# Kernel tuning notes

Hardware: AMD Instinct MI355X
Metric: run time of the kernel (lower is better)

Reference implementation:

```python
import jax, jax.numpy as jnp
import numpy as np

N, E, G = 50000, 800000, 64
L, C, IN, H, OUT = 3, 4, 64, 64, 64
BN_EPS = 1e-5


def setup_inputs() -> dict:
    key = jax.random.key(0)
    ks = jax.random.split(key, 12)
    x = jax.random.normal(ks[0], (N, IN), dtype=jnp.float32)
    cluster_labels = jax.random.randint(ks[1], (N,), 0, C, dtype=jnp.int32)
    edge_index = jax.random.randint(ks[2], (2, E), 0, N, dtype=jnp.int64)
    batch = jnp.sort(jax.random.randint(ks[3], (N,), 0, G, dtype=jnp.int64))
    s1 = 1.0 / np.sqrt(H)
    # per (layer, cluster) GIN MLP params: Lin(H,H) -> BN -> ReLU -> Lin(H,H)
    W1 = jax.random.normal(ks[4], (L, C, H, H), dtype=jnp.float32) * s1
    b1 = jnp.zeros((L, C, H), dtype=jnp.float32)
    g1 = jnp.ones((L, C, H), dtype=jnp.float32)
    be1 = jnp.zeros((L, C, H), dtype=jnp.float32)
    W2 = jax.random.normal(ks[5], (L, C, H, H), dtype=jnp.float32) * s1
    b2 = jnp.zeros((L, C, H), dtype=jnp.float32)
    # pool MLP: Lin(H*L, H) -> BN -> ReLU -> Lin(H, OUT)
    Wp1 = jax.random.normal(ks[6], (H * L, H), dtype=jnp.float32) / np.sqrt(H * L)
    bp1 = jnp.zeros((H,), dtype=jnp.float32)
    gp = jnp.ones((H,), dtype=jnp.float32)
    bep = jnp.zeros((H,), dtype=jnp.float32)
    Wp2 = jax.random.normal(ks[7], (H, OUT), dtype=jnp.float32) * s1
    bp2 = jnp.zeros((OUT,), dtype=jnp.float32)
    return {"x": x, "cluster_labels": cluster_labels, "edge_index": edge_index,
            "batch": batch, "W1": W1, "b1": b1, "g1": g1, "be1": be1,
            "W2": W2, "b2": b2, "Wp1": Wp1, "bp1": bp1, "gp": gp,
            "bep": bep, "Wp2": Wp2, "bp2": bp2}


def _masked_bn(h, mf, gamma, beta):
    # BatchNorm computed only over rows where mask is set (those are the rows fed to nn)
    cnt = jnp.maximum(mf.sum(), 1.0)
    mean = (mf[:, None] * h).sum(0) / cnt
    var = (mf[:, None] * (h - mean) ** 2).sum(0) / cnt
    return (h - mean) * jax.lax.rsqrt(var + BN_EPS) * gamma + beta


def _bn(h, gamma, beta):
    mean = h.mean(0)
    var = ((h - mean) ** 2).mean(0)
    return (h - mean) * jax.lax.rsqrt(var + BN_EPS) * gamma + beta


def reference(x, cluster_labels, edge_index, batch, W1, b1, g1, be1, W2, b2,
              Wp1, bp1, gp, bep, Wp2, bp2):
    src, dst = edge_index[0], edge_index[1]
    pooled = []
    for t in range(L):
        for c in range(C):
            mask = cluster_labels == c
            mf = mask.astype(x.dtype)
            # GIN aggregation: out[i] = sum_{j -> i} x[j]
            agg = jax.ops.segment_sum(x[src], dst, num_segments=N)
            h = agg + x  # (1 + eps) * x residual with eps = 0
            h = h @ W1[t, c] + b1[t, c]
            h = jax.nn.relu(_masked_bn(h, mf, g1[t, c], be1[t, c]))
            h = h @ W2[t, c] + b2[t, c]
            x = jnp.where(mask[:, None], h, x)
        pooled.append(jax.ops.segment_sum(x, batch, num_segments=G))
    z = jnp.concatenate(pooled, axis=1)  # [G, H*L]
    z = z @ Wp1 + bp1
    z = jax.nn.relu(_bn(z, gp, bep))
    return z @ Wp2 + bp2
```

## Files before the change

### kernel.cpp

```cpp
#include <hip/hip_runtime.h>
#include <hip/hip_bf16.h>

#define NN 50000
#define EE 800000
#define GG 64
#define LL 3
#define CC 4
#define HH 64
#define BN_EPS 1e-5f
#define NSHADOW 4
#define SBLK 196
#define GIN_BLOCKS 2048
#define MM_BLOCKS 256
#define ECHUNKS 3125
#define NODE_RANGE 6250


typedef __attribute__((ext_vector_type(8))) short bf16x8;
typedef __attribute__((ext_vector_type(4))) float f32x4;

__device__ __forceinline__ float bf2f(short s) {
    return __int_as_float(((int)(unsigned short)s) << 16);
}
__device__ __forceinline__ short f2bf(float v) {
    __hip_bfloat16 hb = __float2bfloat16(v);
    return *(short*)&hb;
}


__global__ void k_deghist(const int* __restrict__ dst, int* __restrict__ deg,
                          const int* __restrict__ labels, int* __restrict__ blockcnt,
                          const float* __restrict__ x_in, __hip_bfloat16* __restrict__ xw,
                          const float* __restrict__ W1, const float* __restrict__ W2,
                          short* __restrict__ wf) {
    __shared__ int cnt[CC];
    int tid = threadIdx.x;
    for (int i = blockIdx.x * 256 + tid; i < NN * 64; i += gridDim.x * 256)
        xw[i] = __float2bfloat16(x_in[i]);
    int o = blockIdx.x * 256 + tid;
    if (o < 24 * 4096) {
        int m = o >> 12;
        int r = o & 4095;
        int colt = r >> 10;
        int fragk = (r >> 9) & 1;
        int lane = (r >> 3) & 63;
        int j = r & 7;
        int k = fragk * 32 + ((lane >> 4) << 3) + j;
        int n = colt * 16 + (lane & 15);
        const float* src = (m < 12) ? (W1 + (size_t)m * 4096) : (W2 + (size_t)(m - 12) * 4096);
        wf[o] = f2bf(src[k * 64 + n]);
    }
    bool hist = (blockIdx.x < SBLK);
    if (hist && tid < CC) cnt[tid] = 0;
    __syncthreads();
    int gid = blockIdx.x * 256 + tid;
    if (gid < EE) atomicAdd(&deg[dst[gid]], 1);
    if (hist && gid < NN) atomicAdd(&cnt[labels[gid]], 1);
    __syncthreads();
    if (hist && tid < CC) blockcnt[tid * SBLK + blockIdx.x] = cnt[tid];
}

__global__ __launch_bounds__(256) void k_scancombo(
    const int* __restrict__ deg, int* __restrict__ rowptr, int* __restrict__ dpart,
    const int* __restrict__ blockcnt, int* __restrict__ coffs, int* __restrict__ ccount) {
    __shared__ int smem[CC * 256];
    int tid = threadIdx.x;
    if (blockIdx.x < SBLK) {
        int i = blockIdx.x * 256 + tid;
        int v = (i < NN) ? deg[i] : 0;
        smem[tid] = v;
        __syncthreads();
        for (int off = 1; off < 256; off <<= 1) {
            int u = (tid >= off) ? smem[tid - off] : 0;
            __syncthreads();
            smem[tid] += u;
            __syncthreads();
        }
        if (i < NN) rowptr[i] = smem[tid] - v;
        if (tid == 255) dpart[blockIdx.x] = smem[255];
    } else {
        int own[CC];
        for (int c = 0; c < CC; c++) {
            own[c] = (tid < SBLK) ? blockcnt[c * SBLK + tid] : 0;
            smem[c * 256 + tid] = own[c];
        }
        __syncthreads();
        for (int off = 1; off < 256; off <<= 1) {
            int v[CC];
            for (int c = 0; c < CC; c++) v[c] = (tid >= off) ? smem[c * 256 + tid - off] : 0;
            __syncthreads();
            for (int c = 0; c < CC; c++) smem[c * 256 + tid] += v[c];
            __syncthreads();
        }
        if (tid < SBLK)
            for (int c = 0; c < CC; c++) coffs[c * SBLK + tid] = smem[c * 256 + tid] - own[c];
        if (tid == 0)
            for (int c = 0; c < CC; c++) ccount[c] = smem[c * 256 + 255];
    }
}

__global__ __launch_bounds__(256) void k_dscan2(int* __restrict__ dpart,
                                                int* __restrict__ dbase,
                                                int* __restrict__ rowptr) {
    __shared__ int s[256];
    int tid = threadIdx.x;
    int v = (tid < SBLK) ? dpart[tid] : 0;
    s[tid] = v;
    __syncthreads();
    for (int off = 1; off < 256; off <<= 1) {
        int u = (tid >= off) ? s[tid - off] : 0;
        __syncthreads();
        s[tid] += u;
        __syncthreads();
    }
    if (tid < SBLK) dbase[tid] = s[tid] - v;
    if (tid == 0) rowptr[NN] = EE;
}

__global__ __launch_bounds__(256) void k_cfill_dscan3(
    int* __restrict__ rowptr, const int* __restrict__ dbase, int* __restrict__ cursor,
    const int* __restrict__ labels, const int* __restrict__ coffs, int* __restrict__ clist) {
    __shared__ int pos[CC];
    int tid = threadIdx.x;
    if (tid < CC) pos[tid] = coffs[tid * SBLK + blockIdx.x];
    __syncthreads();
    int i = blockIdx.x * 256 + tid;
    if (i < NN) {
        int r = rowptr[i] + dbase[blockIdx.x];
        rowptr[i] = r;
        cursor[i] = r;
        int c = labels[i];
        int p = atomicAdd(&pos[c], 1);
        clist[c * NN + p] = i;
    }
}

__global__ void k_fill(const int* __restrict__ src, const int* __restrict__ dst,
                       int* __restrict__ cursor, int* __restrict__ adj) {
    int range = blockIdx.x / ECHUNKS;
    int e = (blockIdx.x - range * ECHUNKS) * 256 + threadIdx.x;
    if (e < EE) {
        int d = dst[e];
        int lo = range * NODE_RANGE;
        if (d >= lo && d < lo + NODE_RANGE) {
            int pos = atomicAdd(&cursor[d], 1);
            adj[pos] = src[e] << 7;
        }
    }
}

__global__ __launch_bounds__(256) void k_gather(
    const __hip_bfloat16* __restrict__ xw, const int* __restrict__ adj,
    const int* __restrict__ rowptr, const int* __restrict__ clist_c,
    const int* __restrict__ ccount_c, __hip_bfloat16* __restrict__ aggbuf,
    const int* __restrict__ batch, float* __restrict__ z, int tpool) {
    int cnt = *ccount_c;
    int lane = threadIdx.x & 63;
    int wave = threadIdx.x >> 6;
    int wid = blockIdx.x * 4 + wave;
    int nwaves = gridDim.x * 4;
    int grp = lane >> 4;
    int l16 = lane & 15;
    const char* xwb = (const char*)xw;
    int idx = wid;
    int node_next = (idx < cnt) ? clist_c[idx] : 0;
    for (; idx < cnt; idx += nwaves) {
        int node = node_next;
        int nidx = idx + nwaves;
        if (nidx < cnt) node_next = clist_c[nidx];
        int rb = rowptr[node], re = rowptr[node + 1];
        float ax[8], ay[8], az[8], aw[8];
        #pragma unroll
        for (int u = 0; u < 8; u++) { ax[u] = 0.f; ay[u] = 0.f; az[u] = 0.f; aw[u] = 0.f; }
        if (grp == 0) {
            uint2 v = *(const uint2*)(xwb + ((size_t)node << 7) + l16 * 8);
            ax[0] += __int_as_float((int)(v.x << 16));
            ay[0] += __int_as_float((int)(v.x & 0xffff0000u));
            az[0] += __int_as_float((int)(v.y << 16));
            aw[0] += __int_as_float((int)(v.y & 0xffff0000u));
        }
        int base = rb, rem = re - rb;
        while (rem > 0) {
            int take = min(rem, 64);
            int nb = adj[base + min(lane, take - 1)];
            int j = 0;
            for (; j + 32 <= take; j += 32) {
                #pragma unroll
                for (int u = 0; u < 8; u++) {
                    int o = __shfl(nb, j + u * 4 + grp);
                    uint2 v = *(const uint2*)(xwb + o + l16 * 8);
                    ax[u] += __int_as_float((int)(v.x << 16));
                    ay[u] += __int_as_float((int)(v.x & 0xffff0000u));
                    az[u] += __int_as_float((int)(v.y << 16));
                    aw[u] += __int_as_float((int)(v.y & 0xffff0000u));
                }
            }
            for (; j + 16 <= take; j += 16) {
                #pragma unroll
                for (int u = 0; u < 4; u++) {
                    int o = __shfl(nb, j + u * 4 + grp);
                    uint2 v = *(const uint2*)(xwb + o + l16 * 8);
                    ax[u] += __int_as_float((int)(v.x << 16));
                    ay[u] += __int_as_float((int)(v.x & 0xffff0000u));
                    az[u] += __int_as_float((int)(v.y << 16));
                    aw[u] += __int_as_float((int)(v.y & 0xffff0000u));
                }
            }
            for (; j < take; j += 4) {
                int e = j + grp;
                int o = __shfl(nb, min(e, take - 1));
                if (e < take) {
                    uint2 v = *(const uint2*)(xwb + o + l16 * 8);
                    ax[0] += __int_as_float((int)(v.x << 16));
                    ay[0] += __int_as_float((int)(v.x & 0xffff0000u));
                    az[0] += __int_as_float((int)(v.y << 16));
                    aw[0] += __int_as_float((int)(v.y & 0xffff0000u));
                }
            }
            base += take; rem -= take;
        }
        float X = ((ax[0] + ax[1]) + (ax[2] + ax[3])) + ((ax[4] + ax[5]) + (ax[6] + ax[7]));
        float Y = ((ay[0] + ay[1]) + (ay[2] + ay[3])) + ((ay[4] + ay[5]) + (ay[6] + ay[7]));
        float Z = ((az[0] + az[1]) + (az[2] + az[3])) + ((az[4] + az[5]) + (az[6] + az[7]));
        float W = ((aw[0] + aw[1]) + (aw[2] + aw[3])) + ((aw[4] + aw[5]) + (aw[6] + aw[7]));
        X += __shfl_xor(X, 16); X += __shfl_xor(X, 32);
        Y += __shfl_xor(Y, 16); Y += __shfl_xor(Y, 32);
        Z += __shfl_xor(Z, 16); Z += __shfl_xor(Z, 32);
        W += __shfl_xor(W, 16); W += __shfl_xor(W, 32);
        if (grp == 0) {
            ushort4 st;
            st.x = (unsigned short)f2bf(X);
            st.y = (unsigned short)f2bf(Y);
            st.z = (unsigned short)f2bf(Z);
            st.w = (unsigned short)f2bf(W);
            *(ushort4*)((char*)aggbuf + ((size_t)idx << 7) + l16 * 8) = st;
        }
    }
    if (tpool >= 0) {
        int lo = wid * 64;
        if (lo < NN) {
            int hi = min(lo + 64, NN);
            float acc = 0.f;
            int curg = batch[lo];
            for (int n = lo; n < hi; n++) {
                int g = batch[n];
                if (g != curg) {
                    atomicAdd(&z[curg * (HH * LL) + tpool * HH + lane], acc);
                    acc = 0.f;
                    curg = g;
                }
                acc += __bfloat162float(xw[(size_t)n * 64 + lane]);
            }
            atomicAdd(&z[curg * (HH * LL) + tpool * HH + lane], acc);
        }
    }
}

__global__ __launch_bounds__(256) void k_lin1(
    const __hip_bfloat16* __restrict__ aggbuf, const int* __restrict__ ccount_c,
    const short* __restrict__ wf1, const float* __restrict__ b1c,
    __hip_bfloat16* __restrict__ h1buf, float* __restrict__ bnacc) {
    int cnt = *ccount_c;
    int tiles = (cnt + 15) >> 4;
    int lane = threadIdx.x & 63;
    int wave = threadIdx.x >> 6;
    int wid = blockIdx.x * 4 + wave;
    int nwaves = gridDim.x * 4;
    int quad = lane >> 4;
    int l15 = lane & 15;

    bf16x8 wb[8];
    #pragma unroll
    for (int f = 0; f < 8; f++)
        wb[f] = *(const bf16x8*)(wf1 + f * 512 + lane * 8);
    float bcol[4];
    #pragma unroll
    for (int colt = 0; colt < 4; colt++) bcol[colt] = b1c[colt * 16 + l15];

    float sS[4] = {0.f, 0.f, 0.f, 0.f};
    float sQ[4] = {0.f, 0.f, 0.f, 0.f};

    for (int tile = wid; tile < tiles; tile += nwaves) {
        int tb = tile << 4;
        int row = tb + l15;
        const __hip_bfloat16* ar = aggbuf + (size_t)row * 64 + quad * 8;
        bf16x8 a0 = *(const bf16x8*)ar;
        bf16x8 a1 = *(const bf16x8*)(ar + 32);
        #pragma unroll
        for (int colt = 0; colt < 4; colt++) {
            f32x4 acc = {0.f, 0.f, 0.f, 0.f};
            acc = __builtin_amdgcn_mfma_f32_16x16x32_bf16(a0, wb[colt * 2 + 0], acc, 0, 0, 0);
            acc = __builtin_amdgcn_mfma_f32_16x16x32_bf16(a1, wb[colt * 2 + 1], acc, 0, 0, 0);
            #pragma unroll
            for (int r = 0; r < 4; r++) {
                int nrow = tb + quad * 4 + r;
                if (nrow < cnt) {
                    float s = acc[r] + bcol[colt];
                    __hip_bfloat16 hb = __float2bfloat16(s);
                    h1buf[(size_t)nrow * 64 + colt * 16 + l15] = hb;
                    float st = __bfloat162float(hb);
                    sS[colt] += st;
                    sQ[colt] += st * st;
                }
            }
        }
    }
    #pragma unroll
    for (int colt = 0; colt < 4; colt++) {
        sS[colt] += __shfl_xor(sS[colt], 16); sS[colt] += __shfl_xor(sS[colt], 32);
        sQ[colt] += __shfl_xor(sQ[colt], 16); sQ[colt] += __shfl_xor(sQ[colt], 32);
    }
    if (quad == 0) {
        int slot = (blockIdx.x & (NSHADOW - 1)) * 128;
        #pragma unroll
        for (int colt = 0; colt < 4; colt++) {
            atomicAdd(&bnacc[slot + colt * 16 + l15], sS[colt]);
            atomicAdd(&bnacc[slot + 64 + colt * 16 + l15], sQ[colt]);
        }
    }
}

__global__ __launch_bounds__(256) void k_cmfma(
    __hip_bfloat16* __restrict__ xw, const int* __restrict__ clist_c,
    const int* __restrict__ ccount_c, const float* __restrict__ g1c,
    const float* __restrict__ be1c, const short* __restrict__ wf2,
    const float* __restrict__ b2c, const __hip_bfloat16* __restrict__ h1buf,
    const float* __restrict__ bnacc) {
    __shared__ float lds_scale[64];
    __shared__ float lds_shift[64];
    int cnt = *ccount_c;
    int tiles = (cnt + 15) >> 4;
    int lane = threadIdx.x & 63;
    int wave = threadIdx.x >> 6;
    int wid = blockIdx.x * 4 + wave;
    int nwaves = gridDim.x * 4;
    int quad = lane >> 4;
    int l15 = lane & 15;

    if (threadIdx.x < 64) {
        float s = 0.f, q = 0.f;
        #pragma unroll
        for (int sh = 0; sh < NSHADOW; sh++) {
            s += bnacc[sh * 128 + threadIdx.x];
            q += bnacc[sh * 128 + 64 + threadIdx.x];
        }
        float fc = fmaxf((float)cnt, 1.f);
        float mean = s / fc;
        float var = q / fc - mean * mean;
        float sc = g1c[threadIdx.x] * rsqrtf(var + BN_EPS);
        lds_scale[threadIdx.x] = sc;
        lds_shift[threadIdx.x] = be1c[threadIdx.x] - mean * sc;
    }
    __syncthreads();

    bf16x8 wb[8];
    #pragma unroll
    for (int f = 0; f < 8; f++)
        wb[f] = *(const bf16x8*)(wf2 + f * 512 + lane * 8);
    float bcol[4];
    #pragma unroll
    for (int colt = 0; colt < 4; colt++) bcol[colt] = b2c[colt * 16 + l15];
    float scl0[8], sft0[8], scl1[8], sft1[8];
    #pragma unroll
    for (int j = 0; j < 8; j++) {
        int ch = quad * 8 + j;
        scl0[j] = lds_scale[ch];      sft0[j] = lds_shift[ch];
        scl1[j] = lds_scale[ch + 32]; sft1[j] = lds_shift[ch + 32];
    }

    for (int tile = wid; tile < tiles; tile += nwaves) {
        int tb = tile << 4;
        int row = tb + l15;
        const __hip_bfloat16* hr = h1buf + (size_t)row * 64 + quad * 8;
        bf16x8 h0 = *(const bf16x8*)hr;
        bf16x8 h1f = *(const bf16x8*)(hr + 32);
        bf16x8 a0, a1;
        #pragma unroll
        for (int j = 0; j < 8; j++) {
            a0[j] = f2bf(fmaxf(bf2f(h0[j]) * scl0[j] + sft0[j], 0.f));
            a1[j] = f2bf(fmaxf(bf2f(h1f[j]) * scl1[j] + sft1[j], 0.f));
        }
        #pragma unroll
        for (int colt = 0; colt < 4; colt++) {
            f32x4 acc = {0.f, 0.f, 0.f, 0.f};
            acc = __builtin_amdgcn_mfma_f32_16x16x32_bf16(a0, wb[colt * 2 + 0], acc, 0, 0, 0);
            acc = __builtin_amdgcn_mfma_f32_16x16x32_bf16(a1, wb[colt * 2 + 1], acc, 0, 0, 0);
            #pragma unroll
            for (int r = 0; r < 4; r++) {
                int nrow = tb + quad * 4 + r;
                if (nrow < cnt) {
                    int node = clist_c[nrow];
                    xw[(size_t)node * 64 + colt * 16 + l15] =
                        __float2bfloat16(acc[r] + bcol[colt]);
                }
            }
        }
    }
}

__global__ void k_pool(const __hip_bfloat16* __restrict__ xw, const int* __restrict__ batch,
                       float* __restrict__ z, int t) {
    const int CHUNK = 64;
    int lane = threadIdx.x & 63;
    int wg = (blockIdx.x * blockDim.x + threadIdx.x) >> 6;
    int lo = wg * CHUNK;
    if (lo >= NN) return;
    int hi = min(lo + CHUNK, NN);
    float acc = 0.f;
    int curg = batch[lo];
    for (int n = lo; n < hi; n++) {
        int g = batch[n];
        if (g != curg) {
            atomicAdd(&z[curg * (HH * LL) + t * HH + lane], acc);
            acc = 0.f;
            curg = g;
        }
        acc += __bfloat162float(xw[(size_t)n * 64 + lane]);
    }
    atomicAdd(&z[curg * (HH * LL) + t * HH + lane], acc);
}

__global__ __launch_bounds__(256) void k_final1(
    const float* __restrict__ z, const float* __restrict__ Wp1,
    const float* __restrict__ bp1, float* __restrict__ hbuf) {
    __shared__ float red[256];
    int g = blockIdx.x;
    int k = threadIdx.x & 63;
    int part = threadIdx.x >> 6;
    float s = 0.f;
    #pragma unroll 8
    for (int j = part * 48; j < (part + 1) * 48; j++)
        s += z[g * (HH * LL) + j] * Wp1[j * 64 + k];
    red[threadIdx.x] = s;
    __syncthreads();
    if (part == 0)
        hbuf[g * 64 + k] = red[k] + red[64 + k] + red[128 + k] + red[192 + k] + bp1[k];
}

__global__ __launch_bounds__(256) void k_final2(
    const float* __restrict__ hbuf, const float* __restrict__ gp,
    const float* __restrict__ bep, const float* __restrict__ Wp2,
    const float* __restrict__ bp2, float* __restrict__ out) {
    __shared__ float lds[64 * 64];
    __shared__ float sscale[64];
    __shared__ float sshift[64];
    int tid = threadIdx.x;
    for (int i = tid; i < 64 * 64; i += 256) lds[i] = hbuf[i];
    __syncthreads();
    if (tid < 64) {
        float s = 0.f, q = 0.f;
        for (int g = 0; g < 64; g++) { float v = lds[g * 64 + tid]; s += v; q += v * v; }
        float mean = s / 64.f;
        float var = q / 64.f - mean * mean;
        float sc = gp[tid] * rsqrtf(var + BN_EPS);
        sscale[tid] = sc;
        sshift[tid] = bep[tid] - mean * sc;
    }
    __syncthreads();
    for (int i = tid; i < 64 * 64; i += 256) {
        int k = i & 63;
        lds[i] = fmaxf(lds[i] * sscale[k] + sshift[k], 0.f);
    }
    __syncthreads();
    for (int i = tid; i < 64 * 64; i += 256) {
        int g = i >> 6, o = i & 63;
        float s = bp2[o];
        #pragma unroll 8
        for (int k = 0; k < 64; k++) s += lds[g * 64 + k] * Wp2[k * 64 + o];
        out[g * 64 + o] = s;
    }
}

extern "C" void kernel_launch(void* const* d_in, const int* in_sizes, int n_in,
                              void* d_out, int out_size, void* d_ws, size_t ws_size,
                              hipStream_t stream) {
    const float* x_in = (const float*)d_in[0];
    const int* labels = (const int*)d_in[1];
    const int* esrc = (const int*)d_in[2];
    const int* edst = esrc + EE;
    const int* batch = (const int*)d_in[3];
    const float* W1 = (const float*)d_in[4];
    const float* b1 = (const float*)d_in[5];
    const float* g1 = (const float*)d_in[6];
    const float* be1 = (const float*)d_in[7];
    const float* W2 = (const float*)d_in[8];
    const float* b2 = (const float*)d_in[9];
    const float* Wp1 = (const float*)d_in[10];
    const float* bp1 = (const float*)d_in[11];
    const float* gp = (const float*)d_in[12];
    const float* bep = (const float*)d_in[13];
    const float* Wp2 = (const float*)d_in[14];
    const float* bp2 = (const float*)d_in[15];
    float* out = (float*)d_out;

    char* p = (char*)d_ws;
    auto carve = [&](size_t bytes) -> void* {
        void* r = (void*)p;
        p += (bytes + 255) & ~(size_t)255;
        return r;
    };
    float* bnacc = (float*)carve((size_t)LL * CC * NSHADOW * 128 * 4);
    float* z     = (float*)carve((size_t)GG * HH * LL * 4);
    int*   deg   = (int*)carve((size_t)NN * 4);
    size_t zero_bytes = (size_t)(p - (char*)d_ws);
    int*   ccount  = (int*)carve(CC * 4);
    int*   blockcnt= (int*)carve((size_t)CC * SBLK * 4);
    int*   coffs   = (int*)carve((size_t)CC * SBLK * 4);
    int*   dpart   = (int*)carve((size_t)SBLK * 4);
    int*   dbase   = (int*)carve((size_t)SBLK * 4);
    __hip_bfloat16* xw     = (__hip_bfloat16*)carve((size_t)NN * 64 * 2);
    __hip_bfloat16* aggbuf = (__hip_bfloat16*)carve((size_t)NN * 64 * 2);
    __hip_bfloat16* h1buf  = (__hip_bfloat16*)carve((size_t)NN * 64 * 2);
    short* wf      = (short*)carve((size_t)24 * 4096 * 2);
    float* hbuf    = (float*)carve((size_t)GG * 64 * 4);
    int*   rowptr  = (int*)carve((size_t)(NN + 1) * 4);
    int*   cursor  = (int*)carve((size_t)NN * 4);
    int*   adj     = (int*)carve((size_t)EE * 4);
    int*   clist   = (int*)carve((size_t)CC * NN * 4);

    hipMemsetAsync(d_ws, 0, zero_bytes, stream);

    k_deghist<<<ECHUNKS, 256, 0, stream>>>(edst, deg, labels, blockcnt, x_in, xw, W1, W2, wf);
    k_scancombo<<<SBLK + 1, 256, 0, stream>>>(deg, rowptr, dpart, blockcnt, coffs, ccount);
    k_dscan2<<<1, 256, 0, stream>>>(dpart, dbase, rowptr);
    k_cfill_dscan3<<<SBLK, 256, 0, stream>>>(rowptr, dbase, cursor, labels, coffs, clist);
    k_fill<<<ECHUNKS * 8, 256, 0, stream>>>(esrc, edst, cursor, adj);

    for (int t = 0; t < LL; t++) {
        for (int c = 0; c < CC; c++) {
            int tc = t * CC + c;
            int tpool = (c == 0) ? (t - 1) : -1;
            k_gather<<<GIN_BLOCKS, 256, 0, stream>>>(
                xw, adj, rowptr, clist + c * NN, ccount + c, aggbuf, batch, z, tpool);
            k_lin1<<<MM_BLOCKS, 256, 0, stream>>>(
                aggbuf, ccount + c, wf + (size_t)tc * 4096, b1 + (size_t)tc * 64,
                h1buf, bnacc + (size_t)tc * NSHADOW * 128);
            k_cmfma<<<MM_BLOCKS, 256, 0, stream>>>(
                xw, clist + c * NN, ccount + c,
                g1 + (size_t)tc * 64, be1 + (size_t)tc * 64,
                wf + (size_t)(12 + tc) * 4096, b2 + (size_t)tc * 64,
                h1buf, bnacc + (size_t)tc * NSHADOW * 128);
        }
    }
    {
        int pool_waves = (NN + 63) / 64;
        int pool_blocks = (pool_waves * 64 + 255) / 256;
        k_pool<<<pool_blocks, 256, 0, stream>>>(xw, batch, z, LL - 1);
    }
    k_final1<<<GG, 256, 0, stream>>>(z, Wp1, bp1, hbuf);
    k_final2<<<1, 256, 0, stream>>>(hbuf, gp, bep, Wp2, bp2, out);
}
```

Baseline: 554.7 us.

## Fuse neighbor gather with first GIN linear layer and BN stats

```diff
diff --git a/kernel.cpp b/kernel.cpp
--- a/kernel.cpp
+++ b/kernel.cpp
@@ -149,11 +149,14 @@
     }
 }
 
-__global__ __launch_bounds__(256) void k_gather(
+__global__ __launch_bounds__(256) void k_gl1(
     const __hip_bfloat16* __restrict__ xw, const int* __restrict__ adj,
     const int* __restrict__ rowptr, const int* __restrict__ clist_c,
-    const int* __restrict__ ccount_c, __hip_bfloat16* __restrict__ aggbuf,
+    const int* __restrict__ ccount_c, const short* __restrict__ wf1,
+    const float* __restrict__ b1c, __hip_bfloat16* __restrict__ h1buf,
+    float* __restrict__ bnacc,
     const int* __restrict__ batch, float* __restrict__ z, int tpool) {
+    __shared__ float lds_red[4][128];
     int cnt = *ccount_c;
     int lane = threadIdx.x & 63;
     int wave = threadIdx.x >> 6;
@@ -162,6 +165,18 @@
     int grp = lane >> 4;
     int l16 = lane & 15;
     const char* xwb = (const char*)xw;
+
+    bf16x8 wb[8];
+    #pragma unroll
+    for (int f = 0; f < 8; f++)
+        wb[f] = *(const bf16x8*)(wf1 + f * 512 + lane * 8);
+    float bcol[4];
+    #pragma unroll
+    for (int colt = 0; colt < 4; colt++) bcol[colt] = b1c[colt * 16 + l16];
+
+    float sS[4] = {0.f, 0.f, 0.f, 0.f};
+    float sQ[4] = {0.f, 0.f, 0.f, 0.f};
+
     int idx = wid;
     int node_next = (idx < cnt) ? clist_c[idx] : 0;
     for (; idx < cnt; idx += nwaves) {
@@ -169,9 +184,9 @@
         int nidx = idx + nwaves;
         if (nidx < cnt) node_next = clist_c[nidx];
         int rb = rowptr[node], re = rowptr[node + 1];
-        float ax[8], ay[8], az[8], aw[8];
+        float ax[4], ay[4], az[4], aw[4];
         #pragma unroll
-        for (int u = 0; u < 8; u++) { ax[u] = 0.f; ay[u] = 0.f; az[u] = 0.f; aw[u] = 0.f; }
+        for (int u = 0; u < 4; u++) { ax[u] = 0.f; ay[u] = 0.f; az[u] = 0.f; aw[u] = 0.f; }
         if (grp == 0) {
             uint2 v = *(const uint2*)(xwb + ((size_t)node << 7) + l16 * 8);
             ax[0] += __int_as_float((int)(v.x << 16));
@@ -184,17 +199,6 @@
             int take = min(rem, 64);
             int nb = adj[base + min(lane, take - 1)];
             int j = 0;
-            for (; j + 32 <= take; j += 32) {
-                #pragma unroll
-                for (int u = 0; u < 8; u++) {
-                    int o = __shfl(nb, j + u * 4 + grp);
-                    uint2 v = *(const uint2*)(xwb + o + l16 * 8);
-                    ax[u] += __int_as_float((int)(v.x << 16));
-                    ay[u] += __int_as_float((int)(v.x & 0xffff0000u));
-                    az[u] += __int_as_float((int)(v.y << 16));
-                    aw[u] += __int_as_float((int)(v.y & 0xffff0000u));
-                }
-            }
             for (; j + 16 <= take; j += 16) {
                 #pragma unroll
                 for (int u = 0; u < 4; u++) {
@@ -219,22 +223,54 @@
             }
             base += take; rem -= take;
         }
-        float X = ((ax[0] + ax[1]) + (ax[2] + ax[3])) + ((ax[4] + ax[5]) + (ax[6] + ax[7]));
-        float Y = ((ay[0] + ay[1]) + (ay[2] + ay[3])) + ((ay[4] + ay[5]) + (ay[6] + ay[7]));
-        float Z = ((az[0] + az[1]) + (az[2] + az[3])) + ((az[4] + az[5]) + (az[6] + az[7]));
-        float W = ((aw[0] + aw[1]) + (aw[2] + aw[3])) + ((aw[4] + aw[5]) + (aw[6] + aw[7]));
+        float X = (ax[0] + ax[1]) + (ax[2] + ax[3]);
+        float Y = (ay[0] + ay[1]) + (ay[2] + ay[3]);
+        float Z = (az[0] + az[1]) + (az[2] + az[3]);
+        float W = (aw[0] + aw[1]) + (aw[2] + aw[3]);
         X += __shfl_xor(X, 16); X += __shfl_xor(X, 32);
         Y += __shfl_xor(Y, 16); Y += __shfl_xor(Y, 32);
         Z += __shfl_xor(Z, 16); Z += __shfl_xor(Z, 32);
         W += __shfl_xor(W, 16); W += __shfl_xor(W, 32);
-        if (grp == 0) {
-            ushort4 st;
-            st.x = (unsigned short)f2bf(X);
-            st.y = (unsigned short)f2bf(Y);
-            st.z = (unsigned short)f2bf(Z);
-            st.w = (unsigned short)f2bf(W);
-            *(ushort4*)((char*)aggbuf + ((size_t)idx << 7) + l16 * 8) = st;
-        }
+        bf16x8 a0, a1;
+        {
+            int s0 = grp * 2, s1 = grp * 2 + 1;
+            a0[0] = f2bf(__shfl(X, s0)); a0[1] = f2bf(__shfl(Y, s0));
+            a0[2] = f2bf(__shfl(Z, s0)); a0[3] = f2bf(__shfl(W, s0));
+            a0[4] = f2bf(__shfl(X, s1)); a0[5] = f2bf(__shfl(Y, s1));
+            a0[6] = f2bf(__shfl(Z, s1)); a0[7] = f2bf(__shfl(W, s1));
+            int s2 = 8 + grp * 2, s3 = 8 + grp * 2 + 1;
+            a1[0] = f2bf(__shfl(X, s2)); a1[1] = f2bf(__shfl(Y, s2));
+            a1[2] = f2bf(__shfl(Z, s2)); a1[3] = f2bf(__shfl(W, s2));
+            a1[4] = f2bf(__shfl(X, s3)); a1[5] = f2bf(__shfl(Y, s3));
+            a1[6] = f2bf(__shfl(Z, s3)); a1[7] = f2bf(__shfl(W, s3));
+        }
+        #pragma unroll
+        for (int colt = 0; colt < 4; colt++) {
+            f32x4 acc = {0.f, 0.f, 0.f, 0.f};
+            acc = __builtin_amdgcn_mfma_f32_16x16x32_bf16(a0, wb[colt * 2 + 0], acc, 0, 0, 0);
+            acc = __builtin_amdgcn_mfma_f32_16x16x32_bf16(a1, wb[colt * 2 + 1], acc, 0, 0, 0);
+            if (grp == 0) {
+                float s = acc[0] + bcol[colt];
+                short hb = f2bf(s);
+                h1buf[(size_t)idx * 64 + colt * 16 + l16] = *(__hip_bfloat16*)&hb;
+                float st = bf2f(hb);
+                sS[colt] += st;
+                sQ[colt] += st * st;
+            }
+        }
+    }
+    if (grp == 0) {
+        #pragma unroll
+        for (int colt = 0; colt < 4; colt++) {
+            lds_red[wave][colt * 16 + l16] = sS[colt];
+            lds_red[wave][64 + colt * 16 + l16] = sQ[colt];
+        }
+    }
+    __syncthreads();
+    if (threadIdx.x < 128) {
+        float v = lds_red[0][threadIdx.x] + lds_red[1][threadIdx.x] +
+                  lds_red[2][threadIdx.x] + lds_red[3][threadIdx.x];
+        atomicAdd(&bnacc[(blockIdx.x & (NSHADOW - 1)) * 128 + threadIdx.x], v);
     }
     if (tpool >= 0) {
         int lo = wid * 64;
@@ -252,70 +288,6 @@
                 acc += __bfloat162float(xw[(size_t)n * 64 + lane]);
             }
             atomicAdd(&z[curg * (HH * LL) + tpool * HH + lane], acc);
-        }
-    }
-}
-
-__global__ __launch_bounds__(256) void k_lin1(
-    const __hip_bfloat16* __restrict__ aggbuf, const int* __restrict__ ccount_c,
-    const short* __restrict__ wf1, const float* __restrict__ b1c,
-    __hip_bfloat16* __restrict__ h1buf, float* __restrict__ bnacc) {
-    int cnt = *ccount_c;
-    int tiles = (cnt + 15) >> 4;
-    int lane = threadIdx.x & 63;
-    int wave = threadIdx.x >> 6;
-    int wid = blockIdx.x * 4 + wave;
-    int nwaves = gridDim.x * 4;
-    int quad = lane >> 4;
-    int l15 = lane & 15;
-
-    bf16x8 wb[8];
-    #pragma unroll
-    for (int f = 0; f < 8; f++)
-        wb[f] = *(const bf16x8*)(wf1 + f * 512 + lane * 8);
-    float bcol[4];
-    #pragma unroll
-    for (int colt = 0; colt < 4; colt++) bcol[colt] = b1c[colt * 16 + l15];
-
-    float sS[4] = {0.f, 0.f, 0.f, 0.f};
-    float sQ[4] = {0.f, 0.f, 0.f, 0.f};
-
-    for (int tile = wid; tile < tiles; tile += nwaves) {
-        int tb = tile << 4;
-        int row = tb + l15;
-        const __hip_bfloat16* ar = aggbuf + (size_t)row * 64 + quad * 8;
-        bf16x8 a0 = *(const bf16x8*)ar;
-        bf16x8 a1 = *(const bf16x8*)(ar + 32);
-        #pragma unroll
-        for (int colt = 0; colt < 4; colt++) {
-            f32x4 acc = {0.f, 0.f, 0.f, 0.f};
-            acc = __builtin_amdgcn_mfma_f32_16x16x32_bf16(a0, wb[colt * 2 + 0], acc, 0, 0, 0);
-            acc = __builtin_amdgcn_mfma_f32_16x16x32_bf16(a1, wb[colt * 2 + 1], acc, 0, 0, 0);
-            #pragma unroll
-            for (int r = 0; r < 4; r++) {
-                int nrow = tb + quad * 4 + r;
-                if (nrow < cnt) {
-                    float s = acc[r] + bcol[colt];
-                    __hip_bfloat16 hb = __float2bfloat16(s);
-                    h1buf[(size_t)nrow * 64 + colt * 16 + l15] = hb;
-                    float st = __bfloat162float(hb);
-                    sS[colt] += st;
-                    sQ[colt] += st * st;
-                }
-            }
-        }
-    }
-    #pragma unroll
-    for (int colt = 0; colt < 4; colt++) {
-        sS[colt] += __shfl_xor(sS[colt], 16); sS[colt] += __shfl_xor(sS[colt], 32);
-        sQ[colt] += __shfl_xor(sQ[colt], 16); sQ[colt] += __shfl_xor(sQ[colt], 32);
-    }
-    if (quad == 0) {
-        int slot = (blockIdx.x & (NSHADOW - 1)) * 128;
-        #pragma unroll
-        for (int colt = 0; colt < 4; colt++) {
-            atomicAdd(&bnacc[slot + colt * 16 + l15], sS[colt]);
-            atomicAdd(&bnacc[slot + 64 + colt * 16 + l15], sQ[colt]);
         }
     }
 }
@@ -508,9 +480,8 @@
     int*   coffs   = (int*)carve((size_t)CC * SBLK * 4);
     int*   dpart   = (int*)carve((size_t)SBLK * 4);
     int*   dbase   = (int*)carve((size_t)SBLK * 4);
-    __hip_bfloat16* xw     = (__hip_bfloat16*)carve((size_t)NN * 64 * 2);
-    __hip_bfloat16* aggbuf = (__hip_bfloat16*)carve((size_t)NN * 64 * 2);
-    __hip_bfloat16* h1buf  = (__hip_bfloat16*)carve((size_t)NN * 64 * 2);
+    __hip_bfloat16* xw    = (__hip_bfloat16*)carve((size_t)NN * 64 * 2);
+    __hip_bfloat16* h1buf = (__hip_bfloat16*)carve((size_t)NN * 64 * 2);
     short* wf      = (short*)carve((size_t)24 * 4096 * 2);
     float* hbuf    = (float*)carve((size_t)GG * 64 * 4);
     int*   rowptr  = (int*)carve((size_t)(NN + 1) * 4);
@@ -530,11 +501,10 @@
         for (int c = 0; c < CC; c++) {
             int tc = t * CC + c;
             int tpool = (c == 0) ? (t - 1) : -1;
-            k_gather<<<GIN_BLOCKS, 256, 0, stream>>>(
-                xw, adj, rowptr, clist + c * NN, ccount + c, aggbuf, batch, z, tpool);
-            k_lin1<<<MM_BLOCKS, 256, 0, stream>>>(
-                aggbuf, ccount + c, wf + (size_t)tc * 4096, b1 + (size_t)tc * 64,
-                h1buf, bnacc + (size_t)tc * NSHADOW * 128);
+            k_gl1<<<GIN_BLOCKS, 256, 0, stream>>>(
+                xw, adj, rowptr, clist + c * NN, ccount + c,
+                wf + (size_t)tc * 4096, b1 + (size_t)tc * 64, h1buf,
+                bnacc + (size_t)tc * NSHADOW * 128, batch, z, tpool);
             k_cmfma<<<MM_BLOCKS, 256, 0, stream>>>(
                 xw, clist + c * NN, ccount + c,
                 g1 + (size_t)tc * 64, be1 + (size_t)tc * 64,
```

After: 601.3 us. +8.4%, slower.
